# Performance work log

Hardware: AMD Instinct MI355X
Metric: run time of the kernel (lower is better)

Reference implementation:

```python
import jax, jax.numpy as jnp
import numpy as np

B, N, NE = 16, 96, 256
ATOM, EDIM, HID, LAT, HEADS = 128, 16, 128, 128, 4
HD = LAT // HEADS
RBF, CUT, ZEMB, MAXZ = 16, 5.0, 32, 100
MUL0_IN, MUL1_IN = 64, 32      # irreps_node = 64x0e + 32x1o (dim 160)
MUL0_OUT, MUL1_OUT = 32, 16    # out irreps  = 32x0e + 16x1o (dim 80)
NODE_DIM = MUL0_IN + 3 * MUL1_IN
OUT_DIM = MUL0_OUT + 3 * MUL1_OUT
E_ATT = 1024
WNUM = MUL0_IN*MUL0_OUT + MUL0_IN*MUL1_OUT + MUL1_IN*MUL1_OUT + MUL1_IN*MUL0_OUT  # 4608


def _mlp3(x, w1, b1, w2, b2, w3, b3):
    x = jax.nn.silu(x @ w1 + b1)
    x = jax.nn.silu(x @ w2 + b2)
    return x @ w3 + b3


def setup_inputs() -> dict:
    key = jax.random.key(0)
    ks = jax.random.split(key, 40)
    s = 0.05  # scale params so deep MLP activations stay numerically sane
    d = {}
    d['h'] = jax.random.normal(ks[0], (B, N, ATOM), jnp.float32)
    d['h_full'] = jax.random.normal(ks[1], (B, N, NODE_DIM), jnp.float32)
    d['e_feat'] = jax.random.normal(ks[2], (NE, EDIM), jnp.float32)
    d['att_dist'] = jax.random.uniform(ks[3], (E_ATT,), jnp.float32)
    d['att_vec'] = jax.random.normal(ks[4], (E_ATT, 3), jnp.float32)
    d['z_emb_table'] = jax.random.normal(ks[5], (MAXZ + 1, ZEMB), jnp.float32) * s
    d['rw1'] = jax.random.normal(ks[6], (ZEMB + 1 + RBF, HID), jnp.float32) * s
    d['rb1'] = jnp.zeros((HID,), jnp.float32)
    d['rw2'] = jax.random.normal(ks[7], (HID, WNUM), jnp.float32) * s
    d['rb2'] = jnp.zeros((WNUM,), jnp.float32)
    d['ew1'] = jax.random.normal(ks[8], (EDIM, HID), jnp.float32) * s
    d['eb1'] = jnp.zeros((HID,), jnp.float32)
    d['ew2'] = jax.random.normal(ks[9], (HID, MUL0_OUT + MUL1_OUT), jnp.float32) * s
    d['eb2'] = jnp.zeros((MUL0_OUT + MUL1_OUT,), jnp.float32)
    d['qw1'] = jax.random.normal(ks[10], (ATOM + EDIM, HID), jnp.float32) * s
    d['qb1'] = jnp.zeros((HID,), jnp.float32)
    d['qw2'] = jax.random.normal(ks[11], (HID, HID), jnp.float32) * s
    d['qb2'] = jnp.zeros((HID,), jnp.float32)
    d['qw3'] = jax.random.normal(ks[12], (HID, LAT), jnp.float32) * s
    d['qb3'] = jnp.zeros((LAT,), jnp.float32)
    d['kw1'] = jax.random.normal(ks[13], (ATOM + ZEMB + 1 + RBF, HID), jnp.float32) * s
    d['kb1'] = jnp.zeros((HID,), jnp.float32)
    d['kw2'] = jax.random.normal(ks[14], (HID, HID), jnp.float32) * s
    d['kb2'] = jnp.zeros((HID,), jnp.float32)
    d['kw3'] = jax.random.normal(ks[15], (HID, LAT), jnp.float32) * s
    d['kb3'] = jnp.zeros((LAT,), jnp.float32)
    d['ow1'] = jax.random.normal(ks[16], (MUL0_OUT + MUL1_OUT, HID), jnp.float32) * s
    d['ob1'] = jnp.zeros((HID,), jnp.float32)
    d['ow2'] = jax.random.normal(ks[17], (HID, HID), jnp.float32) * s
    d['ob2'] = jnp.zeros((HID,), jnp.float32)
    d['ow3'] = jax.random.normal(ks[18], (HID, LAT), jnp.float32) * s
    d['ob3'] = jnp.zeros((LAT,), jnp.float32)
    d['z'] = jax.random.randint(ks[19], (B, N), 0, MAXZ)
    d['mask'] = jnp.ones((B, N), bool)
    d['absorber_index'] = jax.random.randint(ks[20], (B,), 0, N)
    d['att_dst'] = jnp.arange(E_ATT)  # unique flat indices into B*N
    return d


def reference(h, h_full, e_feat, att_dist, att_vec, z_emb_table,
              rw1, rb1, rw2, rb2, ew1, eb1, ew2, eb2,
              qw1, qb1, qw2, qb2, qw3, qb3,
              kw1, kb1, kw2, kb2, kw3, kb3,
              ow1, ob1, ow2, ob2, ow3, ob3,
              z, mask, absorber_index, att_dst):
    Bz, Na, Hd = h.shape
    F = Bz * Na
    nE = e_feat.shape[0]
    # scatter edge data into flat (B*N) atom slots
    am_flat = jnp.zeros((F,), bool).at[att_dst].set(True)
    d_flat = jnp.zeros((F,), h.dtype).at[att_dst].set(att_dist)
    v_flat = jnp.zeros((F, 3), h.dtype).at[att_dst].set(att_vec)
    att_mask = am_flat.reshape(Bz, Na) & mask
    # spherical harmonics (lmax=1, component normalization): Y0 = 1, Y1 = sqrt(3)*unit_vec
    un = v_flat / jnp.maximum(jnp.linalg.norm(v_flat, axis=-1, keepdims=True), 1e-8)
    y1 = jnp.sqrt(3.0) * un
    # Gaussian RBF on absorber->atom distance
    mu = jnp.linspace(0.0, CUT, RBF)
    delta = CUT / (RBF - 1)
    rbf = jnp.exp(-(d_flat[:, None] - mu) ** 2 / (2.0 * delta * delta))  # (F, RBF)
    zr = z_emb_table[z]                      # (B, N, ZEMB)
    zr_flat = zr.reshape(F, -1)
    is_abs = jnp.zeros((Bz, Na), h.dtype).at[jnp.arange(Bz), absorber_index].set(1.0)
    # radial MLP -> per-edge tensor-product weights
    w_in = jnp.concatenate([zr_flat, is_abs.reshape(F, 1), rbf], -1)
    tpw = jax.nn.silu(w_in @ rw1 + rb1) @ rw2 + rb2  # (F, WNUM)
    s1 = MUL0_IN * MUL0_OUT
    s2 = s1 + MUL0_IN * MUL1_OUT
    s3 = s2 + MUL1_IN * MUL1_OUT
    w00 = tpw[:, :s1].reshape(F, MUL0_IN, MUL0_OUT)   # 0e x 0e -> 0e
    w01 = tpw[:, s1:s2].reshape(F, MUL0_IN, MUL1_OUT) # 0e x 1o -> 1o
    w10 = tpw[:, s2:s3].reshape(F, MUL1_IN, MUL1_OUT) # 1o x 0e -> 1o
    w11 = tpw[:, s3:].reshape(F, MUL1_IN, MUL0_OUT)   # 1o x 1o -> 0e
    hf = h_full.reshape(F, -1)
    x0 = hf[:, :MUL0_IN]
    x1 = hf[:, MUL0_IN:].reshape(F, MUL1_IN, 3)
    alpha = 1.0 / jnp.sqrt(jnp.float32(MUL0_IN + MUL1_IN))  # path fan-in normalization
    c = 1.0 / jnp.sqrt(3.0)                                  # wigner-3j coeff for l=1 couplings
    out0 = alpha * (jnp.einsum('fi,fio->fo', x0, w00)
                    + c * jnp.einsum('fim,fm,fio->fo', x1, y1, w11))
    out1 = alpha * c * (jnp.einsum('fi,fm,fio->fom', x0, y1, w01)
                        + jnp.einsum('fim,fio->fom', x1, w10))
    v_irrep = jnp.concatenate([out0, out1.reshape(F, 3 * MUL1_OUT)], -1)  # (F, OUT_DIM)
    # cosine cutoff envelope + edge mask
    env = jnp.where(d_flat < CUT, 0.5 * (jnp.cos(jnp.pi * d_flat / CUT) + 1.0), 0.0)
    v_irrep = v_irrep * (am_flat.astype(h.dtype) * env)[:, None]
    # energy-conditioned per-irrep-channel modulation
    gates = jax.nn.silu(e_feat @ ew1 + eb1) @ ew2 + eb2  # (nE, 48)
    g_exp = jnp.concatenate([gates[:, :MUL0_OUT],
                             jnp.repeat(gates[:, MUL0_OUT:], 3, axis=-1)], -1)  # (nE, OUT_DIM)
    v_mod = (v_irrep[:, None, :] * g_exp[None]).reshape(Bz, Na, nE, OUT_DIM)
    # invariant multi-head scoring
    h_abs = h[jnp.arange(Bz), absorber_index]  # (B, H)
    q_in = jnp.concatenate([jnp.broadcast_to(h_abs[:, None], (Bz, nE, Hd)),
                            jnp.broadcast_to(e_feat[None], (Bz, nE, EDIM))], -1)
    q = _mlp3(q_in, qw1, qb1, qw2, qb2, qw3, qb3)  # (B, nE, LAT)
    atom_static = jnp.concatenate([h, zr, is_abs[..., None], rbf.reshape(Bz, Na, RBF)], -1)
    k = _mlp3(atom_static, kw1, kb1, kw2, kb2, kw3, kb3)  # (B, N, LAT)
    qh = q.reshape(Bz, nE, HEADS, HD)
    kh = k.reshape(Bz, Na, HEADS, HD)
    scores = (jnp.einsum('behd,bnhd->benh', qh, kh) * (HD ** -0.5)).mean(-1)  # (B, nE, N)
    m = att_mask[:, None, :]
    scores = jnp.where(m, scores, -1e9)
    attn = jax.nn.softmax(scores, axis=2) * m.astype(h.dtype)
    attn = attn / jnp.maximum(attn.sum(2, keepdims=True), 1e-8)
    out_irrep = jnp.einsum('ben,bnec->bec', attn, v_mod)  # (B, nE, OUT_DIM)
    # invariants: scalars + vector norms
    scal = out_irrep[..., :MUL0_OUT]
    vec = out_irrep[..., MUL0_OUT:].reshape(Bz, nE, MUL1_OUT, 3)
    inv = jnp.concatenate([scal, jnp.sqrt(jnp.sum(vec * vec, -1) + 1e-12)], -1)
    return _mlp3(inv, ow1, ob1, ow2, ob2, ow3, ob3)  # (B, nE, LAT)
```

## Files before the change

kernel.cpp:

```cpp
#include <hip/hip_runtime.h>
#include <hip/hip_fp16.h>
#include <math.h>

#define BB 16
#define NN 96
#define NE 256
#define FF (BB*NN)
#define ATOM 128
#define EDIM 16
#define HID 128
#define LAT 128
#define RBFN 16
#define CUTOFF 5.0f
#define ZEMB 32
#define E_ATT 1024
#define M0I 64
#define M1I 32
#define M0O 32
#define M1O 16
#define NODE_DIM 160
#define OUT_DIM 80
#define INVD 48
#define WNUM 4608

#define K1_TP 192
#define K1_EDGE_AT 192
#define K1_Q_AT 448
#define K1_GATE_AT 960
#define K1_PREP_AT 976
#define K1_BLKS 977

#define CSTR2 520

typedef _Float16 half8_t __attribute__((ext_vector_type(8)));
typedef float float4v __attribute__((ext_vector_type(4)));

__device__ __forceinline__ float silu_f(float x) { return x / (1.0f + expf(-x)); }

__global__ __launch_bounds__(256) void k1(
    const float* __restrict__ h, const float* __restrict__ h_full,
    const float* __restrict__ z_emb, const int* __restrict__ z,
    const int* __restrict__ absorber, const float* __restrict__ e_feat,
    const int* __restrict__ att_dst, const float* __restrict__ att_dist,
    const float* __restrict__ att_vec,
    const float* __restrict__ rw1, const float* __restrict__ rb1,
    const float* __restrict__ rw2, const float* __restrict__ rb2,
    const float* __restrict__ kw1, const float* __restrict__ kb1,
    const float* __restrict__ kw2, const float* __restrict__ kb2,
    const float* __restrict__ kw3, const float* __restrict__ kb3,
    const float* __restrict__ qw1, const float* __restrict__ qb1,
    const float* __restrict__ qw2, const float* __restrict__ qb2,
    const float* __restrict__ qw3, const float* __restrict__ qb3,
    const float* __restrict__ ew1, const float* __restrict__ eb1,
    const float* __restrict__ ew2, const float* __restrict__ eb2,
    float* __restrict__ kmatw, float* __restrict__ qmat,
    float* __restrict__ gexp, float* __restrict__ virr,
    int* __restrict__ inv)
{
    __shared__ __align__(16) char smemraw[36864];
    float* smem = (float*)smemraw;
    int blk = blockIdx.x;
    int t = threadIdx.x;

    if (blk < K1_TP) {
        __half* cS    = (__half*)smemraw;
        float*  fbase = (float*)(smemraw + 16640);
        float* x0f  = fbase;
        float* x1f  = fbase + 1024;
        float* xyf  = fbase + 2560;
        float* y1f  = fbase + 3072;
        float* envf = fbase + 3136;
        float* dS   = fbase + 3152;
        int*   fI   = (int*)(fbase + 3168);
        float* winf = fbase + 3184;
        _Float16* hS = (_Float16*)(smemraw + 32704);

        int cls  = blk % 3;
        int tile = blk / 3;
        int e0t = tile * 16;
        if (t < 16) {
            int e = e0t + t;
            int f = att_dst[e];
            fI[t] = f;
            float d = att_dist[e];
            dS[t] = d;
            envf[t] = (d < CUTOFF) ? 0.5f*(cosf(3.14159265358979323846f*d/CUTOFF) + 1.0f) : 0.0f;
            float vx = att_vec[3*e], vy = att_vec[3*e+1], vz = att_vec[3*e+2];
            float nrm = sqrtf(vx*vx + vy*vy + vz*vz);
            float is = 1.0f / fmaxf(nrm, 1e-8f);
            const float s3 = 1.7320508075688772f;
            y1f[t*4]   = s3*vx*is;
            y1f[t*4+1] = s3*vy*is;
            y1f[t*4+2] = s3*vz*is;
        }
        __syncthreads();
        for (int u = t; u < 16*49; u += 256) {
            int e = u / 49, j = u - 49*(u/49);
            int f = fI[e];
            float v;
            if (j < ZEMB) v = z_emb[z[f]*ZEMB + j];
            else if (j == ZEMB) { int b = f / NN, nn = f - b*NN; v = (absorber[b] == nn) ? 1.0f : 0.0f; }
            else {
                int jr = j - 33;
                const float delta = CUTOFF / (RBFN - 1);
                float diff = dS[e] - jr*delta;
                v = expf(-diff*diff / (2.0f*delta*delta));
            }
            winf[e*52 + j] = v;
        }
        for (int p = 0; p < 10; p++) {
            int idx = t + 256*p;
            int edge = idx / 160, j = idx - 160*edge;
            float v = h_full[fI[edge]*NODE_DIM + j];
            if (j < M0I) x0f[edge*64 + j] = v;
            else         x1f[edge*96 + (j - M0I)] = v;
        }
        __syncthreads();
        for (int p = 0; p < 2; p++) {
            int idx = t + 256*p;
            int edge = idx >> 5, i = idx & 31;
            xyf[edge*32 + i] = x1f[edge*96 + 3*i]*y1f[edge*4]
                             + x1f[edge*96 + 3*i+1]*y1f[edge*4+1]
                             + x1f[edge*96 + 3*i+2]*y1f[edge*4+2];
        }
        {
            int e = t >> 4;
            const float* wf = winf + e*52;
            #pragma unroll
            for (int p = 0; p < 4; p++) {
                int c2 = 2*((t & 15) + 16*p);
                float2 a0 = *(const float2*)&rb1[c2];
                float2 a1 = make_float2(0.f, 0.f);
                #pragma unroll 8
                for (int i = 0; i < 48; i += 2) {
                    float x0v = wf[i], x1v = wf[i + 1];
                    float2 w0 = *(const float2*)&rw1[i*HID + c2];
                    float2 w1 = *(const float2*)&rw1[(i+1)*HID + c2];
                    a0.x += x0v*w0.x; a0.y += x0v*w0.y;
                    a1.x += x1v*w1.x; a1.y += x1v*w1.y;
                }
                {
                    float x0v = wf[48];
                    float2 w0 = *(const float2*)&rw1[48*HID + c2];
                    a0.x += x0v*w0.x; a0.y += x0v*w0.y;
                }
                *(__half2*)&hS[e*128 + c2] =
                    __floats2half2_rn(silu_f(a0.x + a1.x), silu_f(a0.y + a1.y));
            }
        }
        __syncthreads();

        int wv = t >> 6;
        int lane = t & 63;
        int mrow = lane & 15, quad = lane >> 4;
        half8_t af[4];
        #pragma unroll
        for (int kc = 0; kc < 4; kc++)
            af[kc] = *(const half8_t*)&hS[mrow*128 + quad*8 + kc*32];

        int edge = t >> 4, o = t & 15;
        float t00 = 0.f, t11 = 0.f;
        float t01 = 0.f, tm0 = 0.f, tm1 = 0.f, tm2 = 0.f;
        int clsAdd = (cls == 1) ? 1 : 0;

        for (int g = 0; g < 3; g++) {
            #pragma unroll
            for (int jj = 0; jj < 8; jj++) {
                int jl = wv*8 + jj;
                int j = g*32 + jl;
                int ntg = (cls == 2) ? (128 + j)
                                     : (2*j + clsAdd + ((j >= 64) ? 96 : 0));
                const float* bcol = rw2 + ntg*16 + mrow;
                float4v acc = {0.f, 0.f, 0.f, 0.f};
                #pragma unroll
                for (int kc = 0; kc < 4; kc++) {
                    half8_t bfr;
                    #pragma unroll
                    for (int m = 0; m < 8; m++)
                        bfr[m] = (_Float16)bcol[(quad*8 + kc*32 + m)*WNUM];
                    acc = __builtin_amdgcn_mfma_f32_16x16x32_f16(af[kc], bfr, acc, 0, 0, 0);
                }
                float bias = rb2[ntg*16 + mrow];
                #pragma unroll
                for (int r = 0; r < 4; r++)
                    cS[(quad*4 + r)*CSTR2 + jl*16 + mrow] = __float2half(acc[r] + bias);
            }
            __syncthreads();
            const __half* cRow = cS + edge*CSTR2 + o;
            if (cls < 2) {
                if (g < 2) {
                    #pragma unroll 8
                    for (int jl = 0; jl < 32; jl++)
                        t00 += x0f[edge*64 + g*32 + jl]*__half2float(cRow[jl*16]);
                } else {
                    #pragma unroll 8
                    for (int jl = 0; jl < 32; jl++)
                        t11 += xyf[edge*32 + jl]*__half2float(cRow[jl*16]);
                }
            } else {
                if (g < 2) {
                    #pragma unroll 8
                    for (int jl = 0; jl < 32; jl++)
                        t01 += x0f[edge*64 + g*32 + jl]*__half2float(cRow[jl*16]);
                } else {
                    #pragma unroll 8
                    for (int jl = 0; jl < 32; jl++) {
                        float C = __half2float(cRow[jl*16]);
                        tm0 += x1f[edge*96 + 3*jl]*C;
                        tm1 += x1f[edge*96 + 3*jl+1]*C;
                        tm2 += x1f[edge*96 + 3*jl+2]*C;
                    }
                }
            }
            __syncthreads();
        }
        const float alpha = 0.10206207261596575f;
        const float ccf   = 0.5773502691896258f;
        int f = fI[edge];
        float env = envf[edge];
        if (cls < 2) {
            virr[f*OUT_DIM + cls*16 + o] = alpha*(t00 + ccf*t11)*env;
        } else {
            float y0 = y1f[edge*4], y1v = y1f[edge*4+1], y2 = y1f[edge*4+2];
            virr[f*OUT_DIM + M0O + 3*o]     = alpha*ccf*(t01*y0 + tm0)*env;
            virr[f*OUT_DIM + M0O + 3*o + 1] = alpha*ccf*(t01*y1v + tm1)*env;
            virr[f*OUT_DIM + M0O + 3*o + 2] = alpha*ccf*(t01*y2 + tm2)*env;
        }
    } else if (blk < K1_Q_AT) {
        float (*sin1)[184] = (float(*)[184])smem;
        float (*l1S)[128]  = (float(*)[128])(smem + 736);
        float (*l2S)[128]  = (float(*)[128])(smem + 736 + 512);
        int w = t >> 6;
        int c = t & 63;
        int e = (blk - K1_EDGE_AT)*4 + w;
        int f = att_dst[e];
        int b = f / NN, nn = f - b*NN;
        float d = att_dist[e];
        {
            float2 hv = *(const float2*)&h[f*ATOM + 2*c];
            sin1[w][2*c] = hv.x; sin1[w][2*c + 1] = hv.y;
        }
        if (c < ZEMB) sin1[w][ATOM + c] = z_emb[z[f]*ZEMB + c];
        if (c >= 32 && c < 48) {
            int j = c - 32;
            const float delta = CUTOFF / (RBFN - 1);
            float diff = d - j*delta;
            sin1[w][ATOM + ZEMB + 1 + j] = expf(-diff*diff / (2.0f*delta*delta));
        }
        if (c == 48) sin1[w][ATOM + ZEMB] = (absorber[b] == nn) ? 1.0f : 0.0f;
        __syncthreads();
        int c2 = 2*c;
        {
            float2 a0 = *(const float2*)&kb1[c2];
            float2 a1 = make_float2(0.f, 0.f);
            #pragma unroll 8
            for (int i = 0; i < 176; i += 2) {
                float x0v = sin1[w][i], x1v = sin1[w][i + 1];
                float2 w0 = *(const float2*)&kw1[i*HID + c2];
                float2 w1 = *(const float2*)&kw1[(i+1)*HID + c2];
                a0.x += x0v*w0.x; a0.y += x0v*w0.y;
                a1.x += x1v*w1.x; a1.y += x1v*w1.y;
            }
            {
                float x0v = sin1[w][176];
                float2 w0 = *(const float2*)&kw1[176*HID + c2];
                a0.x += x0v*w0.x; a0.y += x0v*w0.y;
            }
            l1S[w][c2] = silu_f(a0.x + a1.x); l1S[w][c2+1] = silu_f(a0.y + a1.y);
        }
        __syncthreads();
        {
            float2 a0 = *(const float2*)&kb2[c2];
            float2 a1 = make_float2(0.f, 0.f);
            #pragma unroll 8
            for (int i = 0; i < HID; i += 2) {
                float x0v = l1S[w][i], x1v = l1S[w][i + 1];
                float2 w0 = *(const float2*)&kw2[i*HID + c2];
                float2 w1 = *(const float2*)&kw2[(i+1)*HID + c2];
                a0.x += x0v*w0.x; a0.y += x0v*w0.y;
                a1.x += x1v*w1.x; a1.y += x1v*w1.y;
            }
            l2S[w][c2] = silu_f(a0.x + a1.x); l2S[w][c2+1] = silu_f(a0.y + a1.y);
        }
        __syncthreads();
        {
            float2 a0 = *(const float2*)&kb3[c2];
            float2 a1 = make_float2(0.f, 0.f);
            #pragma unroll 8
            for (int i = 0; i < HID; i += 2) {
                float x0v = l2S[w][i], x1v = l2S[w][i + 1];
                float2 w0 = *(const float2*)&kw3[i*HID + c2];
                float2 w1 = *(const float2*)&kw3[(i+1)*HID + c2];
                a0.x += x0v*w0.x; a0.y += x0v*w0.y;
                a1.x += x1v*w1.x; a1.y += x1v*w1.y;
            }
            float2 o; o.x = a0.x + a1.x; o.y = a0.y + a1.y;
            *(float2*)&kmatw[f*HID + c2] = o;
        }
    } else if (blk < K1_GATE_AT) {
        float* hA          = smem;
        float (*ef)[16]    = (float(*)[16])(smem + 128);
        float (*part)[128] = (float(*)[128])(smem + 256);
        float* l1S         = smem + 1280;
        float* l2S         = smem + 2304;
        int idx = blk - K1_Q_AT;
        int r0 = idx * 8;
        int b  = r0 >> 8;
        int e8 = r0 & 255;
        if (t < 32) *(float4*)&hA[t*4] = *(const float4*)&h[(b*NN + absorber[b])*ATOM + t*4];
        if (t >= 128 && t < 256) { int e = (t - 128) >> 4, j = t & 15; ef[e][j] = e_feat[(e8 + e)*EDIM + j]; }
        __syncthreads();
        int r = t >> 5, c0 = (t & 31)*4;
        {
            float4 a0 = make_float4(0,0,0,0);
            int k0 = r*16;
            #pragma unroll
            for (int k = 0; k < 16; k++) {
                float hv = hA[k0 + k];
                float4 w0 = *(const float4*)&qw1[(k0 + k)*HID + c0];
                a0.x += hv*w0.x; a0.y += hv*w0.y; a0.z += hv*w0.z; a0.w += hv*w0.w;
            }
            *(float4*)&part[r][c0] = a0;
        }
        __syncthreads();
        {
            float4 s = *(const float4*)&qb1[c0];
            #pragma unroll
            for (int g = 0; g < 8; g++) {
                float4 pg = *(const float4*)&part[g][c0];
                s.x += pg.x; s.y += pg.y; s.z += pg.z; s.w += pg.w;
            }
            #pragma unroll
            for (int j = 0; j < 16; j++) {
                float a = ef[r][j];
                float4 w0 = *(const float4*)&qw1[(ATOM + j)*HID + c0];
                s.x += a*w0.x; s.y += a*w0.y; s.z += a*w0.z; s.w += a*w0.w;
            }
            l1S[r*128 + c0]   = silu_f(s.x); l1S[r*128 + c0+1] = silu_f(s.y);
            l1S[r*128 + c0+2] = silu_f(s.z); l1S[r*128 + c0+3] = silu_f(s.w);
        }
        __syncthreads();
        {
            float4 a0 = *(const float4*)&qb2[c0];
            float4 a1 = make_float4(0,0,0,0);
            #pragma unroll 8
            for (int i = 0; i < HID; i += 2) {
                float x0v = l1S[r*128 + i], x1v = l1S[r*128 + i+1];
                float4 w0 = *(const float4*)&qw2[i*HID + c0];
                float4 w1 = *(const float4*)&qw2[(i+1)*HID + c0];
                a0.x += x0v*w0.x; a0.y += x0v*w0.y; a0.z += x0v*w0.z; a0.w += x0v*w0.w;
                a1.x += x1v*w1.x; a1.y += x1v*w1.y; a1.z += x1v*w1.z; a1.w += x1v*w1.w;
            }
            l2S[r*128 + c0]   = silu_f(a0.x + a1.x); l2S[r*128 + c0+1] = silu_f(a0.y + a1.y);
            l2S[r*128 + c0+2] = silu_f(a0.z + a1.z); l2S[r*128 + c0+3] = silu_f(a0.w + a1.w);
        }
        __syncthreads();
        {
            float4 a0 = *(const float4*)&qb3[c0];
            float4 a1 = make_float4(0,0,0,0);
            #pragma unroll 8
            for (int i = 0; i < HID; i += 2) {
                float x0v = l2S[r*128 + i], x1v = l2S[r*128 + i+1];
                float4 w0 = *(const float4*)&qw3[i*HID + c0];
                float4 w1 = *(const float4*)&qw3[(i+1)*HID + c0];
                a0.x += x0v*w0.x; a0.y += x0v*w0.y; a0.z += x0v*w0.z; a0.w += x0v*w0.w;
                a1.x += x1v*w1.x; a1.y += x1v*w1.y; a1.z += x1v*w1.z; a1.w += x1v*w1.w;
            }
            float4 o;
            o.x = a0.x + a1.x; o.y = a0.y + a1.y; o.z = a0.z + a1.z; o.w = a0.w + a1.w;
            *(float4*)&qmat[(r0 + r)*LAT + c0] = o;
        }
    } else if (blk < K1_PREP_AT) {
        float (*ef)[16]   = (float(*)[16])smem;
        float (*l1g)[128] = (float(*)[128])(smem + 256);
        float (*gg)[48]   = (float(*)[48])(smem + 256 + 2048);
        int e0 = (blk - K1_GATE_AT) * 16;
        { int e = t >> 4, i = t & 15; ef[e][i] = e_feat[(e0 + e)*EDIM + i]; }
        __syncthreads();
        int r = t >> 4, c0 = (t & 15)*8;
        {
            float4 a0 = *(const float4*)&eb1[c0];
            float4 a1 = *(const float4*)&eb1[c0 + 4];
            #pragma unroll
            for (int i = 0; i < EDIM; i++) {
                float a = ef[r][i];
                float4 w0 = *(const float4*)&ew1[i*HID + c0];
                float4 w1 = *(const float4*)&ew1[i*HID + c0 + 4];
                a0.x += a*w0.x; a0.y += a*w0.y; a0.z += a*w0.z; a0.w += a*w0.w;
                a1.x += a*w1.x; a1.y += a*w1.y; a1.z += a*w1.z; a1.w += a*w1.w;
            }
            l1g[r][c0]   = silu_f(a0.x); l1g[r][c0+1] = silu_f(a0.y);
            l1g[r][c0+2] = silu_f(a0.z); l1g[r][c0+3] = silu_f(a0.w);
            l1g[r][c0+4] = silu_f(a1.x); l1g[r][c0+5] = silu_f(a1.y);
            l1g[r][c0+6] = silu_f(a1.z); l1g[r][c0+7] = silu_f(a1.w);
        }
        __syncthreads();
        for (int u = t; u < 16*48; u += 256) {
            int e = u / 48, j = u - 48*(u/48);
            float acc = eb2[j];
            #pragma unroll 4
            for (int i = 0; i < HID; i++) acc += l1g[e][i]*ew2[i*48 + j];
            gg[e][j] = acc;
        }
        __syncthreads();
        for (int u = t; u < 16*80; u += 256) {
            int e = u / 80, cc = u - 80*(u/80);
            gexp[(e0 + e)*OUT_DIM + cc] = (cc < M0O) ? gg[e][cc] : gg[e][M0O + (cc - M0O)/3];
        }
    } else {
        for (int p = 0; p < 6; p++) inv[t + 256*p] = -1;
        __syncthreads();
        for (int p = 0; p < 4; p++) { int e = t + 256*p; inv[att_dst[e]] = e; }
    }
}

__global__ __launch_bounds__(256) void k_attf(
    const float* __restrict__ qmat, const float* __restrict__ kmat,
    const int* __restrict__ inv,
    const float* __restrict__ virr, const float* __restrict__ gexp,
    const float* __restrict__ ow1, const float* __restrict__ ob1,
    const float* __restrict__ ow2, const float* __restrict__ ob2,
    const float* __restrict__ ow3, const float* __restrict__ ob3,
    float* __restrict__ out)
{
    int b  = blockIdx.x >> 5;
    int e0 = (blockIdx.x & 31) * 8;
    int t = threadIdx.x;
    __shared__ float smem[7936];
    float (*aS)[100]   = (float(*)[100])smem;
    float (*gS)[84]    = (float(*)[84])(smem + 800);
    float (*ocS)[84]   = (float(*)[84])(smem + 1472);
    float* mS          = smem + 2144;
    float (*inS)[INVD] = (float(*)[INVD])(smem + 2240);
    float (*q8)[132]   = (float(*)[132])(smem + 2624);
    float* Kt          = smem + 3680;
    float (*l1S)[HID]  = (float(*)[HID])(smem + 3680);
    float (*l2S)[HID]  = (float(*)[HID])(smem + 3680 + 1024);

    if (t < 160) {
        int el = t / 20, c4 = t - 20*(t/20);
        *(float4*)&gS[el][c4*4] = *(const float4*)&gexp[(e0 + el)*OUT_DIM + c4*4];
    }
    if (t < NN) mS[t] = ((unsigned)inv[b*NN + t] < E_ATT) ? 1.0f : 0.0f;
    {
        int el = t >> 5, i4 = t & 31;
        *(float4*)&q8[el][i4*4] = *(const float4*)&qmat[(b*NE + e0 + el)*LAT + i4*4];
    }

    int el = t >> 5, tn = t & 31;
    float sacc0 = 0.f, sacc1 = 0.f, sacc2 = 0.f;
    #pragma unroll
    for (int nt = 0; nt < 3; nt++) {
        __syncthreads();
        for (int p = 0; p < 4; p++) {
            int idx = t + 256*p; int n = idx >> 5, i4 = idx & 31;
            *(float4*)&Kt[n*133 + i4*4] = *(const float4*)&kmat[(b*NN + nt*32 + n)*LAT + i4*4];
        }
        __syncthreads();
        float acc = 0.f;
        for (int i = 0; i < LAT; i++) acc += q8[el][i]*Kt[tn*133 + i];
        if (nt == 0) sacc0 = acc; else if (nt == 1) sacc1 = acc; else sacc2 = acc;
    }

    {
        const float scale = 0.04419417382415922f;
        int ng = tn;
        float m0 = mS[ng], m1 = mS[ng + 32], m2 = mS[ng + 64];
        float s0 = (m0 != 0.f) ? sacc0*scale : -1e9f;
        float s1 = (m1 != 0.f) ? sacc1*scale : -1e9f;
        float s2 = (m2 != 0.f) ? sacc2*scale : -1e9f;
        float mx = fmaxf(s0, fmaxf(s1, s2));
        #pragma unroll
        for (int off = 1; off < 32; off <<= 1) mx = fmaxf(mx, __shfl_xor(mx, off));
        float e0v = expf(s0 - mx), e1v = expf(s1 - mx), e2v = expf(s2 - mx);
        float sm = e0v + e1v + e2v;
        #pragma unroll
        for (int off = 1; off < 32; off <<= 1) sm += __shfl_xor(sm, off);
        float r = 1.0f / sm;
        float p0 = m0*e0v*r, p1 = m1*e1v*r, p2 = m2*e2v*r;
        float ss = p0 + p1 + p2;
        #pragma unroll
        for (int off = 1; off < 32; off <<= 1) ss += __shfl_xor(ss, off);
        float is = 1.0f / fmaxf(ss, 1e-8f);
        aS[el][ng]      = p0*is;
        aS[el][ng + 32] = p1*is;
        aS[el][ng + 64] = p2*is;
    }
    __syncthreads();

    if (t < 160) {
        int el2 = t / 20, c4 = t - 20*(t/20);
        const float* vp = virr + (long)b*NN*OUT_DIM + c4*4;
        float4 acc = make_float4(0,0,0,0);
        #pragma unroll 4
        for (int n = 0; n < NN; n++) {
            float a = aS[el2][n];
            float4 v = *(const float4*)&vp[n*OUT_DIM];
            acc.x += a*v.x; acc.y += a*v.y; acc.z += a*v.z; acc.w += a*v.w;
        }
        float4 g = *(float4*)&gS[el2][c4*4];
        float4 o; o.x = acc.x*g.x; o.y = acc.y*g.y; o.z = acc.z*g.z; o.w = acc.w*g.w;
        *(float4*)&ocS[el2][c4*4] = o;
    }
    __syncthreads();

    for (int u = t; u < 8*INVD; u += 256) {
        int el2 = u / INVD, j = u - INVD*(u/INVD);
        float val;
        if (j < M0O) val = ocS[el2][j];
        else {
            int o = j - M0O;
            float x = ocS[el2][M0O + 3*o], y = ocS[el2][M0O + 3*o + 1], zz = ocS[el2][M0O + 3*o + 2];
            val = sqrtf(x*x + y*y + zz*zz + 1e-12f);
        }
        inS[el2][j] = val;
    }
    __syncthreads();

    int r = t >> 5, c0 = (t & 31)*4;
    {
        float4 a0 = *(const float4*)&ob1[c0];
        float4 a1 = make_float4(0,0,0,0);
        #pragma unroll 8
        for (int i = 0; i < INVD; i += 2) {
            float x0v = inS[r][i], x1v = inS[r][i+1];
            float4 w0 = *(const float4*)&ow1[i*HID + c0];
            float4 w1 = *(const float4*)&ow1[(i+1)*HID + c0];
            a0.x += x0v*w0.x; a0.y += x0v*w0.y; a0.z += x0v*w0.z; a0.w += x0v*w0.w;
            a1.x += x1v*w1.x; a1.y += x1v*w1.y; a1.z += x1v*w1.z; a1.w += x1v*w1.w;
        }
        l1S[r][c0]   = silu_f(a0.x + a1.x); l1S[r][c0+1] = silu_f(a0.y + a1.y);
        l1S[r][c0+2] = silu_f(a0.z + a1.z); l1S[r][c0+3] = silu_f(a0.w + a1.w);
    }
    __syncthreads();
    {
        float4 a0 = *(const float4*)&ob2[c0];
        float4 a1 = make_float4(0,0,0,0);
        #pragma unroll 8
        for (int i = 0; i < HID; i += 2) {
            float x0v = l1S[r][i], x1v = l1S[r][i+1];
            float4 w0 = *(const float4*)&ow2[i*HID + c0];
            float4 w1 = *(const float4*)&ow2[(i+1)*HID + c0];
            a0.x += x0v*w0.x; a0.y += x0v*w0.y; a0.z += x0v*w0.z; a0.w += x0v*w0.w;
            a1.x += x1v*w1.x; a1.y += x1v*w1.y; a1.z += x1v*w1.z; a1.w += x1v*w1.w;
        }
        l2S[r][c0]   = silu_f(a0.x + a1.x); l2S[r][c0+1] = silu_f(a0.y + a1.y);
        l2S[r][c0+2] = silu_f(a0.z + a1.z); l2S[r][c0+3] = silu_f(a0.w + a1.w);
    }
    __syncthreads();
    {
        float4 a0 = *(const float4*)&ob3[c0];
        float4 a1 = make_float4(0,0,0,0);
        #pragma unroll 8
        for (int i = 0; i < HID; i += 2) {
            float x0v = l2S[r][i], x1v = l2S[r][i+1];
            float4 w0 = *(const float4*)&ow3[i*HID + c0];
            float4 w1 = *(const float4*)&ow3[(i+1)*HID + c0];
            a0.x += x0v*w0.x; a0.y += x0v*w0.y; a0.z += x0v*w0.z; a0.w += x0v*w0.w;
            a1.x += x1v*w1.x; a1.y += x1v*w1.y; a1.z += x1v*w1.z; a1.w += x1v*w1.w;
        }
        float4 o;
        o.x = a0.x + a1.x; o.y = a0.y + a1.y; o.z = a0.z + a1.z; o.w = a0.w + a1.w;
        *(float4*)&out[((b*NE + e0) + r)*LAT + c0] = o;
    }
}

extern "C" void kernel_launch(void* const* d_in, const int* in_sizes, int n_in,
                              void* d_out, int out_size, void* d_ws, size_t ws_size,
                              hipStream_t stream) {
    const float* h        = (const float*)d_in[0];
    const float* h_full   = (const float*)d_in[1];
    const float* e_feat   = (const float*)d_in[2];
    const float* att_dist = (const float*)d_in[3];
    const float* att_vec  = (const float*)d_in[4];
    const float* z_emb    = (const float*)d_in[5];
    const float* rw1 = (const float*)d_in[6];  const float* rb1 = (const float*)d_in[7];
    const float* rw2 = (const float*)d_in[8];  const float* rb2 = (const float*)d_in[9];
    const float* ew1 = (const float*)d_in[10]; const float* eb1 = (const float*)d_in[11];
    const float* ew2 = (const float*)d_in[12]; const float* eb2 = (const float*)d_in[13];
    const float* qw1 = (const float*)d_in[14]; const float* qb1 = (const float*)d_in[15];
    const float* qw2 = (const float*)d_in[16]; const float* qb2 = (const float*)d_in[17];
    const float* qw3 = (const float*)d_in[18]; const float* qb3 = (const float*)d_in[19];
    const float* kw1 = (const float*)d_in[20]; const float* kb1 = (const float*)d_in[21];
    const float* kw2 = (const float*)d_in[22]; const float* kb2 = (const float*)d_in[23];
    const float* kw3 = (const float*)d_in[24]; const float* kb3 = (const float*)d_in[25];
    const float* ow1 = (const float*)d_in[26]; const float* ob1 = (const float*)d_in[27];
    const float* ow2 = (const float*)d_in[28]; const float* ob2 = (const float*)d_in[29];
    const float* ow3 = (const float*)d_in[30]; const float* ob3 = (const float*)d_in[31];
    const int* z        = (const int*)d_in[32];
    const int* absorber = (const int*)d_in[34];
    const int* att_dst  = (const int*)d_in[35];

    float* ws = (float*)d_ws;
    int*   inv     = (int*)ws;
    float* kmat    = ws + 5632;
    float* qmat    = ws + 202240;
    float* gexp    = ws + 726528;
    float* virr    = ws + 747008;

    float* out = (float*)d_out;

    k1<<<K1_BLKS, 256, 0, stream>>>(h, h_full, z_emb, z, absorber, e_feat,
                                    att_dst, att_dist, att_vec,
                                    rw1, rb1, rw2, rb2,
                                    kw1, kb1, kw2, kb2, kw3, kb3,
                                    qw1, qb1, qw2, qb2, qw3, qb3,
                                    ew1, eb1, ew2, eb2,
                                    kmat, qmat, gexp, virr, inv);
    k_attf<<<BB*32, 256, 0, stream>>>(qmat, kmat, inv, virr, gexp,
                                      ow1, ob1, ow2, ob2, ow3, ob3, out);
}
```

Baseline: 211.4 us.

## Shrink k1 tensor-product shared memory by processing smaller column groups

The tensor-product branch of k1 now produces and consumes the MFMA output in 12 groups of 8 column tiles instead of 3 groups of 32. This lets the C staging buffer shrink and alias the winf region, cutting static LDS from 36 KB to about 21 KB so more blocks can be resident per CU. The cost is four times as many __syncthreads rounds in that branch. Separately, the attention score dot product is split into two accumulators with explicit unrolling, and the value-aggregation loop unroll factor is raised from 4 to 8.

```diff
diff --git a/kernel.cpp b/kernel.cpp
--- a/kernel.cpp
+++ b/kernel.cpp
@@ -30,8 +30,6 @@
 #define K1_PREP_AT 976
 #define K1_BLKS 977
 
-#define CSTR2 520
-
 typedef _Float16 half8_t __attribute__((ext_vector_type(8)));
 typedef float float4v __attribute__((ext_vector_type(4)));
 
@@ -57,14 +55,15 @@
     float* __restrict__ gexp, float* __restrict__ virr,
     int* __restrict__ inv)
 {
-    __shared__ __align__(16) char smemraw[36864];
+    __shared__ __align__(16) char smemraw[21248];
     float* smem = (float*)smemraw;
     int blk = blockIdx.x;
     int t = threadIdx.x;
 
     if (blk < K1_TP) {
-        __half* cS    = (__half*)smemraw;
-        float*  fbase = (float*)(smemraw + 16640);
+        __half* cS   = (__half*)smemraw;
+        float*  winf = (float*)smemraw;
+        float*  fbase = (float*)smemraw + 1088;
         float* x0f  = fbase;
         float* x1f  = fbase + 1024;
         float* xyf  = fbase + 2560;
@@ -72,8 +71,7 @@
         float* envf = fbase + 3136;
         float* dS   = fbase + 3152;
         int*   fI   = (int*)(fbase + 3168);
-        float* winf = fbase + 3184;
-        _Float16* hS = (_Float16*)(smemraw + 32704);
+        _Float16* hS = (_Float16*)(smemraw + 17088);
 
         int cls  = blk % 3;
         int tile = blk / 3;
@@ -163,11 +161,11 @@
         float t01 = 0.f, tm0 = 0.f, tm1 = 0.f, tm2 = 0.f;
         int clsAdd = (cls == 1) ? 1 : 0;
 
-        for (int g = 0; g < 3; g++) {
+        for (int g = 0; g < 12; g++) {
             #pragma unroll
-            for (int jj = 0; jj < 8; jj++) {
-                int jl = wv*8 + jj;
-                int j = g*32 + jl;
+            for (int sub = 0; sub < 2; sub++) {
+                int ntl = 2*wv + sub;
+                int j = g*8 + ntl;
                 int ntg = (cls == 2) ? (128 + j)
                                      : (2*j + clsAdd + ((j >= 64) ? 96 : 0));
                 const float* bcol = rw2 + ntg*16 + mrow;
@@ -183,32 +181,33 @@
                 float bias = rb2[ntg*16 + mrow];
                 #pragma unroll
                 for (int r = 0; r < 4; r++)
-                    cS[(quad*4 + r)*CSTR2 + jl*16 + mrow] = __float2half(acc[r] + bias);
+                    cS[(quad*4 + r)*136 + ntl*16 + mrow] = __float2half(acc[r] + bias);
             }
             __syncthreads();
-            const __half* cRow = cS + edge*CSTR2 + o;
+            const __half* cRow = cS + edge*136 + o;
             if (cls < 2) {
-                if (g < 2) {
-                    #pragma unroll 8
-                    for (int jl = 0; jl < 32; jl++)
-                        t00 += x0f[edge*64 + g*32 + jl]*__half2float(cRow[jl*16]);
+                if (g < 8) {
+                    #pragma unroll
+                    for (int nt = 0; nt < 8; nt++)
+                        t00 += x0f[edge*64 + g*8 + nt]*__half2float(cRow[nt*16]);
                 } else {
-                    #pragma unroll 8
-                    for (int jl = 0; jl < 32; jl++)
-                        t11 += xyf[edge*32 + jl]*__half2float(cRow[jl*16]);
+                    #pragma unroll
+                    for (int nt = 0; nt < 8; nt++)
+                        t11 += xyf[edge*32 + (g*8 + nt - 64)]*__half2float(cRow[nt*16]);
                 }
             } else {
-                if (g < 2) {
-                    #pragma unroll 8
-                    for (int jl = 0; jl < 32; jl++)
-                        t01 += x0f[edge*64 + g*32 + jl]*__half2float(cRow[jl*16]);
+                if (g < 8) {
+                    #pragma unroll
+                    for (int nt = 0; nt < 8; nt++)
+                        t01 += x0f[edge*64 + g*8 + nt]*__half2float(cRow[nt*16]);
                 } else {
-                    #pragma unroll 8
-                    for (int jl = 0; jl < 32; jl++) {
-                        float C = __half2float(cRow[jl*16]);
-                        tm0 += x1f[edge*96 + 3*jl]*C;
-                        tm1 += x1f[edge*96 + 3*jl+1]*C;
-                        tm2 += x1f[edge*96 + 3*jl+2]*C;
+                    #pragma unroll
+                    for (int nt = 0; nt < 8; nt++) {
+                        int i = g*8 + nt - 64;
+                        float C = __half2float(cRow[nt*16]);
+                        tm0 += x1f[edge*96 + 3*i]*C;
+                        tm1 += x1f[edge*96 + 3*i+1]*C;
+                        tm2 += x1f[edge*96 + 3*i+2]*C;
                     }
                 }
             }
@@ -457,8 +456,13 @@
             *(float4*)&Kt[n*133 + i4*4] = *(const float4*)&kmat[(b*NN + nt*32 + n)*LAT + i4*4];
         }
         __syncthreads();
-        float acc = 0.f;
-        for (int i = 0; i < LAT; i++) acc += q8[el][i]*Kt[tn*133 + i];
+        float a0 = 0.f, a1 = 0.f;
+        #pragma unroll 16
+        for (int i = 0; i < LAT; i += 2) {
+            a0 += q8[el][i]*Kt[tn*133 + i];
+            a1 += q8[el][i+1]*Kt[tn*133 + i+1];
+        }
+        float acc = a0 + a1;
         if (nt == 0) sacc0 = acc; else if (nt == 1) sacc1 = acc; else sacc2 = acc;
     }
 
@@ -492,7 +496,7 @@
         int el2 = t / 20, c4 = t - 20*(t/20);
         const float* vp = virr + (long)b*NN*OUT_DIM + c4*4;
         float4 acc = make_float4(0,0,0,0);
-        #pragma unroll 4
+        #pragma unroll 8
         for (int n = 0; n < NN; n++) {
             float a = aS[el2][n];
             float4 v = *(const float4*)&vp[n*OUT_DIM];
```

Result: no change. 211.0 us (-0.2%).
